# Performance work log

Hardware: AMD Instinct MI355X
Metric: run time of the kernel (lower is better)

## Reference

```python
import jax, jax.numpy as jnp
import numpy as np
from jax import lax

K_NBR = 9  # K nearest neighbors
R = 2      # shuffle_scale


def pixel_unshuffle(x, r):
    B, C, H, W = x.shape
    x = x.reshape(B, C, H // r, r, W // r, r)
    return x.transpose(0, 1, 3, 5, 2, 4).reshape(B, C * r * r, H // r, W // r)


def pixel_shuffle(x, r):
    B, C, H, W = x.shape
    x = x.reshape(B, C // (r * r), r, r, H, W)
    return x.transpose(0, 1, 4, 2, 5, 3).reshape(B, C // (r * r), H * r, W * r)


def conv2d_same(x, w, b):
    y = lax.conv_general_dilated(x, w, (1, 1), 'SAME',
                                 dimension_numbers=('NCHW', 'OIHW', 'NCHW'))
    return y + b[None, :, None, None]


def convnn_branching_layer(x, idx, wa, ba, wb, bb, wp, bp):
    """Conv2d_ConvNN_Random_Branching with shuffle_pattern='BA'."""
    x = pixel_unshuffle(x, R)                      # (B, C*r^2, H/r, W/r)
    B, C, H, W = x.shape
    T = H * W
    # Branch 1: standard 3x3 conv
    y1 = conv2d_same(x, wa, ba)                    # (B, c1, H, W)
    # Branch 2: ConvNN on K nearest of N random samples
    xt = x.reshape(B, C, T)                        # tokens
    samp = xt[:, :, idx]                           # (B, C, N) random samples
    dots = jnp.einsum('bct,bcn->btn', xt, samp)
    xn = jnp.sum(xt * xt, axis=1)[:, :, None]      # (B, T, 1)
    sn = jnp.sum(samp * samp, axis=1)[:, None, :]  # (B, 1, N)
    dist = xn + sn - 2.0 * dots                    # squared euclidean (B, T, N)
    nbr = lax.top_k(-dist, K_NBR)[1]               # (B, T, K) indices into samples
    # gather neighbor features: (B, C, T*K)
    g = jnp.take_along_axis(samp, nbr.reshape(B, 1, T * K_NBR), axis=2)
    g = g.reshape(B, C, T, K_NBR)
    # Conv1d(kernel=K, stride=K) over stacked neighbors
    y2 = jnp.einsum('bctk,ock->bot', g, wb) + bb[None, :, None]
    y2 = y2.reshape(B, wb.shape[0], H, W)          # (B, c2, H, W)
    y = jax.nn.relu(jnp.concatenate([y1, y2], axis=1))
    y = conv2d_same(y, wp, bp)                     # 1x1 -> out*r^2 channels
    return pixel_shuffle(y, R)                     # (B, out, H*r, W*r)


def setup_inputs() -> dict:
    key = jax.random.key(0)
    ks = jax.random.split(key, 24)
    s = 0.02
    B = 256
    inp = {
        'x': jax.random.normal(ks[0], (B, 3, 32, 32), jnp.float32),
        'idx1': jax.random.randint(ks[1], (64,), 0, 256, jnp.int32),
        'idx2': jax.random.randint(ks[2], (64,), 0, 256, jnp.int32),
        # layer 1: Cin = 3*4 = 12, branches 16+16, out 16*4 = 64 pre-shuffle
        'w1a': jax.random.normal(ks[3], (16, 12, 3, 3), jnp.float32) * s,
        'b1a': jnp.zeros((16,), jnp.float32),
        'w1b': jax.random.normal(ks[4], (16, 12, 9), jnp.float32) * s,
        'b1b': jnp.zeros((16,), jnp.float32),
        'w1p': jax.random.normal(ks[5], (64, 32, 1, 1), jnp.float32) * s,
        'b1p': jnp.zeros((64,), jnp.float32),
        # layer 2: Cin = 16*4 = 64, branches 32+32, out 32*4 = 128 pre-shuffle
        'w2a': jax.random.normal(ks[6], (32, 64, 3, 3), jnp.float32) * s,
        'b2a': jnp.zeros((32,), jnp.float32),
        'w2b': jax.random.normal(ks[7], (32, 64, 9), jnp.float32) * s,
        'b2b': jnp.zeros((32,), jnp.float32),
        'w2p': jax.random.normal(ks[8], (128, 64, 1, 1), jnp.float32) * s,
        'b2p': jnp.zeros((128,), jnp.float32),
        # FC head
        'fc1w': jax.random.normal(ks[9], (1024, 32768), jnp.float32) * s,
        'fc1b': jnp.zeros((1024,), jnp.float32),
        'fc2w': jax.random.normal(ks[10], (10, 1024), jnp.float32) * s,
        'fc2b': jnp.zeros((10,), jnp.float32),
    }
    return inp


def reference(x, idx1, idx2, w1a, b1a, w1b, b1b, w1p, b1p,
              w2a, b2a, w2b, b2b, w2p, b2p, fc1w, fc1b, fc2w, fc2b):
    h = convnn_branching_layer(x, idx1, w1a, b1a, w1b, b1b, w1p, b1p)  # (B,16,32,32)
    h = convnn_branching_layer(h, idx2, w2a, b2a, w2b, b2b, w2p, b2p)  # (B,32,32,32)
    h = h.reshape(h.shape[0], -1)                   # (B, 32768)
    h = jax.nn.relu(h @ fc1w.T + fc1b)
    return h @ fc2w.T + fc2b                        # (B, num_classes)
```

## Files before the change

### kernel.cpp

```cpp
#include <hip/hip_runtime.h>
#include <cstdint>
#include <cstddef>


#define DI static __device__ __forceinline__

typedef __attribute__((ext_vector_type(8))) short short8;
typedef __attribute__((ext_vector_type(4))) float f32x4;

DI unsigned short f2bf(float v) {
  unsigned u = __builtin_bit_cast(unsigned, v);
  unsigned r = (u + 0x7FFFu + ((u >> 16) & 1u)) >> 16;
  return (unsigned short)r;
}
DI float bf2f(unsigned short h) {
  unsigned u = ((unsigned)h) << 16;
  return __builtin_bit_cast(float, u);
}

DI float xu1_at(const float* __restrict__ x, int b, int c, int t) {
  int h = t >> 4, w = t & 15;
  return x[(((size_t)b * 3 + (c >> 2)) * 32 + 2 * h + ((c >> 1) & 1)) * 32 + 2 * w + (c & 1)];
}

template <int CIN, bool GATHER, int CCTOT>
__global__ __launch_bounds__(256) void k_conv3x3(
    const float* __restrict__ xsrc, const float* __restrict__ xu,
    const float* __restrict__ w, const float* __restrict__ bias,
    float* __restrict__ ycat)
{
  int b = blockIdx.x;
  int ocb = blockIdx.y * 16;
  __shared__ float xs[CIN * 256];
  int t = threadIdx.x;
  if (GATHER) {
    for (int i = t; i < CIN * 256; i += 256) {
      int c = i >> 8, tt = i & 255;
      xs[i] = xu1_at(xsrc, b, c, tt);
    }
  } else {
    for (int i = t; i < CIN * 256; i += 256) xs[i] = xu[(size_t)b * CIN * 256 + i];
  }
  __syncthreads();
  int h = t >> 4, wc = t & 15;
  float acc[16];
#pragma unroll
  for (int o = 0; o < 16; ++o) acc[o] = bias[ocb + o];
  bool vh0 = h > 0, vh2 = h < 15, vw0 = wc > 0, vw2 = wc < 15;
  bool vm[9] = {vh0 && vw0, vh0, vh0 && vw2, vw0, true, vw2, vh2 && vw0, vh2, vh2 && vw2};
  int tcl[9];
#pragma unroll
  for (int dh = 0; dh < 3; ++dh)
#pragma unroll
    for (int dw = 0; dw < 3; ++dw) {
      int off = (h + dh - 1) * 16 + (wc + dw - 1);
      off = off < 0 ? 0 : (off > 255 ? 255 : off);
      tcl[dh * 3 + dw] = off;
    }
#pragma unroll 2
  for (int ic = 0; ic < CIN; ++ic) {
    float xv[9];
#pragma unroll
    for (int tp = 0; tp < 9; ++tp) {
      float v = xs[ic * 256 + tcl[tp]];
      xv[tp] = vm[tp] ? v : 0.f;
    }
#pragma unroll
    for (int o = 0; o < 16; ++o) {
      const float* wp = w + ((size_t)(ocb + o) * CIN + ic) * 9;
#pragma unroll
      for (int tp = 0; tp < 9; ++tp) acc[o] = fmaf(xv[tp], wp[tp], acc[o]);
    }
  }
#pragma unroll
  for (int o = 0; o < 16; ++o)
    ycat[((size_t)b * CCTOT + ocb + o) * 256 + t] = fmaxf(acc[o], 0.f);
}

__global__ __launch_bounds__(256) void k_prepw(
    const float* __restrict__ w1b, float* __restrict__ wT1,
    const float* __restrict__ w2b, float* __restrict__ wT2)
{
  int t = threadIdx.x;
  for (int i = t; i < 9 * 12 * 16; i += 256) {
    int k = i / (12 * 16), r = i % (12 * 16), c = r >> 4, o = r & 15;
    wT1[i] = w1b[((size_t)o * 12 + c) * 9 + k];
  }
  for (int i = t; i < 9 * 64 * 32; i += 256) {
    int k = i / (64 * 32), r = i % (64 * 32), c = r >> 5, o = r & 31;
    wT2[i] = w2b[((size_t)o * 64 + c) * 9 + k];
  }
}

template <int C, int STR, bool GATHER>
__global__ __launch_bounds__(64) void k_prep(
    const float* __restrict__ xsrc, const float* __restrict__ xu,
    const int* __restrict__ idx,
    float* __restrict__ sampT, float* __restrict__ samp_cn,
    float* __restrict__ snvg)
{
  int b = blockIdx.x, n = threadIdx.x;
  int p = idx[n];
  float s;
  {
#pragma clang fp contract(off)
    s = 0.f;
    for (int c = 0; c < C; ++c) {
      float v = GATHER ? xu1_at(xsrc, b, c, p) : xu[((size_t)b * C + c) * 256 + p];
      sampT[((size_t)b * 64 + n) * STR + c] = v;
      samp_cn[((size_t)b * C + c) * 64 + n] = v;
      s += v * v;
    }
  }
  snvg[(size_t)b * 64 + n] = s;
}

template <int C, int STR, bool GATHER>
__global__ __launch_bounds__(256) void k_nbr(
    const float* __restrict__ xsrc, const float* __restrict__ xu,
    const float* __restrict__ sampT, const float* __restrict__ snvg,
    int* __restrict__ nbr)
{
  int b = blockIdx.x, t = threadIdx.x;
  float xcol[C];
#pragma unroll
  for (int c = 0; c < C; ++c)
    xcol[c] = GATHER ? xu1_at(xsrc, b, c, t) : xu[((size_t)b * C + c) * 256 + t];
  float xn;
  {
#pragma clang fp contract(off)
    xn = 0.f;
#pragma unroll
    for (int c = 0; c < C; ++c) xn += xcol[c] * xcol[c];
  }
  float bd[9];
  int bn[9];
#pragma unroll
  for (int i = 0; i < 9; ++i) { bd[i] = __builtin_inff(); bn[i] = 1 << 30; }

#pragma unroll 1
  for (int n = 0; n < 64; ++n) {
    const float* sp = sampT + ((size_t)b * 64 + n) * STR;
    float snvn = snvg[(size_t)b * 64 + n];
    float d;
    {
#pragma clang fp contract(off)
      float dot = 0.f;
#pragma unroll
      for (int c = 0; c < C; ++c) dot = fmaf(xcol[c], sp[c], dot);
      d = (xn + snvn) - 2.f * dot;
    }
    if (d < bd[8] || (d == bd[8] && n < bn[8])) {
      float dc = d;
      int nc = n;
#pragma unroll
      for (int i = 0; i < 9; ++i) {
        bool sw = (dc < bd[i]) || (dc == bd[i] && nc < bn[i]);
        float ob = bd[i]; int on = bn[i];
        bd[i] = sw ? dc : ob; bn[i] = sw ? nc : on;
        dc = sw ? ob : dc;   nc = sw ? on : nc;
      }
    }
  }
#pragma unroll
  for (int k = 0; k < 9; ++k) nbr[((size_t)b * 9 + k) * 256 + t] = bn[k];
}

template <int C, int OGRP, int OTOT, int CCTOT, int OCBASE>
__global__ __launch_bounds__(256) void k_einsum(
    const float* __restrict__ samp_cn,
    const int* __restrict__ nbr,
    const float* __restrict__ wT,
    const float* __restrict__ bb,
    float* __restrict__ ycat)
{
  int b = blockIdx.x, og = blockIdx.y * OGRP, t = threadIdx.x;
  __shared__ float samps[C * 64];
  for (int i = t; i < C * 64; i += 256)
    samps[i] = samp_cn[(size_t)b * C * 64 + i];
  int bn[9];
#pragma unroll
  for (int k = 0; k < 9; ++k) bn[k] = nbr[((size_t)b * 9 + k) * 256 + t];
  __syncthreads();
  float acc[OGRP];
#pragma unroll
  for (int o = 0; o < OGRP; ++o) acc[o] = bb[og + o];
#pragma unroll 1
  for (int k = 0; k < 9; ++k) {
    int n = bn[k];
    const float* wp = wT + (size_t)k * C * OTOT + og;
#pragma unroll 4
    for (int c = 0; c < C; ++c) {
      float sv = samps[c * 64 + n];
#pragma unroll
      for (int o = 0; o < OGRP; ++o)
        acc[o] = fmaf(sv, wp[c * OTOT + o], acc[o]);
    }
  }
#pragma unroll
  for (int o = 0; o < OGRP; ++o)
    ycat[((size_t)b * CCTOT + OCBASE + og + o) * 256 + t] = fmaxf(acc[o], 0.f);
}

template <int CIN, int OCB, int OCTOT, bool SHUF>
__global__ __launch_bounds__(256) void k_conv1x1(
    const float* __restrict__ yin, const float* __restrict__ w,
    const float* __restrict__ bias, float* __restrict__ out)
{
  int b = blockIdx.x, ocb = blockIdx.y * OCB, t = threadIdx.x;
  __shared__ float ys[CIN * 256];
  for (int i = t; i < CIN * 256; i += 256) ys[i] = yin[(size_t)b * CIN * 256 + i];
  __syncthreads();
  float acc[OCB];
#pragma unroll
  for (int o = 0; o < OCB; ++o) acc[o] = bias[ocb + o];
#pragma unroll 4
  for (int ic = 0; ic < CIN; ++ic) {
    float xv = ys[ic * 256 + t];
#pragma unroll
    for (int o = 0; o < OCB; ++o)
      acc[o] = fmaf(xv, w[(size_t)(ocb + o) * CIN + ic], acc[o]);
  }
  int h = t >> 4, wc = t & 15;
#pragma unroll
  for (int o = 0; o < OCB; ++o) {
    int og = ocb + o;
    if (SHUF) {
      int flat = (og >> 2) * 1024 + (2 * h + ((og >> 1) & 1)) * 32 + (2 * wc + (og & 1));
      out[(size_t)b * 32768 + flat] = acc[o];
    } else {
      out[((size_t)b * OCTOT + og) * 256 + t] = acc[o];
    }
  }
}

__global__ __launch_bounds__(256, 2) void k_fc1(
    const float* __restrict__ A, const float* __restrict__ W,
    float* __restrict__ parts)
{
  constexpr int KTOT = 32768;
  constexpr int LDT = 40;
  __shared__ unsigned short Ah[128 * LDT], Am[128 * LDT], Al[128 * LDT];
  __shared__ unsigned short Wh[128 * LDT], Wm[128 * LDT], Wl[128 * LDT];
  int t = threadIdx.x;
  int nb = blockIdx.x, mb = blockIdx.y, sb = blockIdx.z;
  int m0 = mb * 128, n0 = nb * 128, k0 = sb * 1024;
  int wave = t >> 6, lane = t & 63;
  int q = lane >> 4, m16 = lane & 15;

  f32x4 acc[8][2];
#pragma unroll
  for (int mt = 0; mt < 8; ++mt)
#pragma unroll
    for (int nt = 0; nt < 2; ++nt) acc[mt][nt] = (f32x4){0.f, 0.f, 0.f, 0.f};

  int r8 = t >> 3, c4 = t & 7;

  for (int ks = 0; ks < 1024; ks += 32) {
    int kb = k0 + ks;
    float4 av[4], wv[4];
#pragma unroll
    for (int i = 0; i < 4; ++i) {
      av[i] = *(const float4*)(A + (size_t)(m0 + r8 + 32 * i) * KTOT + kb + c4 * 4);
      wv[i] = *(const float4*)(W + (size_t)(n0 + r8 + 32 * i) * KTOT + kb + c4 * 4);
    }
    __syncthreads();
#pragma unroll
    for (int i = 0; i < 4; ++i) {
      int off = (r8 + 32 * i) * LDT + c4 * 4;
      float vv[4] = {av[i].x, av[i].y, av[i].z, av[i].w};
      ushort4 h4, m4, l4;
      {
        float v = vv[0]; h4.x = f2bf(v); float r1 = v - bf2f(h4.x);
        m4.x = f2bf(r1); l4.x = f2bf(r1 - bf2f(m4.x));
      }
      {
        float v = vv[1]; h4.y = f2bf(v); float r1 = v - bf2f(h4.y);
        m4.y = f2bf(r1); l4.y = f2bf(r1 - bf2f(m4.y));
      }
      {
        float v = vv[2]; h4.z = f2bf(v); float r1 = v - bf2f(h4.z);
        m4.z = f2bf(r1); l4.z = f2bf(r1 - bf2f(m4.z));
      }
      {
        float v = vv[3]; h4.w = f2bf(v); float r1 = v - bf2f(h4.w);
        m4.w = f2bf(r1); l4.w = f2bf(r1 - bf2f(m4.w));
      }
      *(ushort4*)&Ah[off] = h4; *(ushort4*)&Am[off] = m4; *(ushort4*)&Al[off] = l4;
      float uu[4] = {wv[i].x, wv[i].y, wv[i].z, wv[i].w};
      {
        float v = uu[0]; h4.x = f2bf(v); float r1 = v - bf2f(h4.x);
        m4.x = f2bf(r1); l4.x = f2bf(r1 - bf2f(m4.x));
      }
      {
        float v = uu[1]; h4.y = f2bf(v); float r1 = v - bf2f(h4.y);
        m4.y = f2bf(r1); l4.y = f2bf(r1 - bf2f(m4.y));
      }
      {
        float v = uu[2]; h4.z = f2bf(v); float r1 = v - bf2f(h4.z);
        m4.z = f2bf(r1); l4.z = f2bf(r1 - bf2f(m4.z));
      }
      {
        float v = uu[3]; h4.w = f2bf(v); float r1 = v - bf2f(h4.w);
        m4.w = f2bf(r1); l4.w = f2bf(r1 - bf2f(m4.w));
      }
      *(ushort4*)&Wh[off] = h4; *(ushort4*)&Wm[off] = m4; *(ushort4*)&Wl[off] = l4;
    }
    __syncthreads();
    short8 bh[2], bm[2], bl[2];
#pragma unroll
    for (int nt = 0; nt < 2; ++nt) {
      int boff = (wave * 32 + nt * 16 + m16) * LDT + q * 8;
      bh[nt] = *(const short8*)&Wh[boff];
      bm[nt] = *(const short8*)&Wm[boff];
      bl[nt] = *(const short8*)&Wl[boff];
    }
#pragma unroll
    for (int mt = 0; mt < 8; ++mt) {
      int aoff = (mt * 16 + m16) * LDT + q * 8;
      short8 ah = *(const short8*)&Ah[aoff];
      short8 am = *(const short8*)&Am[aoff];
      short8 al = *(const short8*)&Al[aoff];
#pragma unroll
      for (int nt = 0; nt < 2; ++nt) {
        acc[mt][nt] = __builtin_amdgcn_mfma_f32_16x16x32_bf16(al, bh[nt], acc[mt][nt], 0, 0, 0);
        acc[mt][nt] = __builtin_amdgcn_mfma_f32_16x16x32_bf16(am, bm[nt], acc[mt][nt], 0, 0, 0);
        acc[mt][nt] = __builtin_amdgcn_mfma_f32_16x16x32_bf16(ah, bl[nt], acc[mt][nt], 0, 0, 0);
        acc[mt][nt] = __builtin_amdgcn_mfma_f32_16x16x32_bf16(am, bh[nt], acc[mt][nt], 0, 0, 0);
        acc[mt][nt] = __builtin_amdgcn_mfma_f32_16x16x32_bf16(ah, bm[nt], acc[mt][nt], 0, 0, 0);
        acc[mt][nt] = __builtin_amdgcn_mfma_f32_16x16x32_bf16(ah, bh[nt], acc[mt][nt], 0, 0, 0);
      }
    }
  }
  float* P = parts + (size_t)sb * 262144;
#pragma unroll
  for (int mt = 0; mt < 8; ++mt)
#pragma unroll
    for (int nt = 0; nt < 2; ++nt)
#pragma unroll
      for (int r2 = 0; r2 < 4; ++r2) {
        int m = m0 + mt * 16 + q * 4 + r2;
        int n = n0 + wave * 32 + nt * 16 + m16;
        P[(size_t)m * 1024 + n] = acc[mt][nt][r2];
      }
}

__global__ __launch_bounds__(256) void k_fc1_reduce(const float* __restrict__ parts,
                                                    const float* __restrict__ bias,
                                                    float* __restrict__ h1) {
  int i = blockIdx.x * 256 + threadIdx.x;
  float s = 0.f;
#pragma unroll
  for (int sb = 0; sb < 32; ++sb) s += parts[(size_t)sb * 262144 + i];
  h1[i] = fmaxf(s + bias[i & 1023], 0.f);
}

__global__ __launch_bounds__(256) void k_fc2(const float* __restrict__ h1,
                                             const float* __restrict__ w,
                                             const float* __restrict__ bias,
                                             float* __restrict__ out)
{
  int m = blockIdx.x, tid = threadIdx.x;
  __shared__ float hs[1024];
  __shared__ float ps[256];
  for (int i = tid; i < 1024; i += 256) hs[i] = h1[(size_t)m * 1024 + i];
  __syncthreads();
  int n = tid >> 4, sl = tid & 15;
  float p = 0.f;
  if (n < 10) {
    const float* wr = w + (size_t)n * 1024 + sl * 64;
    const float* hr = hs + sl * 64;
#pragma unroll 8
    for (int j = 0; j < 64; ++j) p = fmaf(hr[j], wr[j], p);
  }
  ps[tid] = p;
  __syncthreads();
  if (sl == 0 && n < 10) {
    float s = 0.f;
#pragma unroll
    for (int q = 0; q < 16; ++q) s += ps[n * 16 + q];
    out[(size_t)m * 10 + n] = s + bias[n];
  }
}

extern "C" void kernel_launch(void* const* d_in, const int* in_sizes, int n_in,
                              void* d_out, int out_size, void* d_ws, size_t ws_size,
                              hipStream_t stream) {
  (void)in_sizes; (void)n_in; (void)out_size; (void)ws_size;
  const float* x    = (const float*)d_in[0];
  const int*   idx1 = (const int*)d_in[1];
  const int*   idx2 = (const int*)d_in[2];
  const float* w1a  = (const float*)d_in[3];
  const float* b1a  = (const float*)d_in[4];
  const float* w1b  = (const float*)d_in[5];
  const float* b1b  = (const float*)d_in[6];
  const float* w1p  = (const float*)d_in[7];
  const float* b1p  = (const float*)d_in[8];
  const float* w2a  = (const float*)d_in[9];
  const float* b2a  = (const float*)d_in[10];
  const float* w2b  = (const float*)d_in[11];
  const float* b2b  = (const float*)d_in[12];
  const float* w2p  = (const float*)d_in[13];
  const float* b2p  = (const float*)d_in[14];
  const float* fc1w = (const float*)d_in[15];
  const float* fc1b = (const float*)d_in[16];
  const float* fc2w = (const float*)d_in[17];
  const float* fc2b = (const float*)d_in[18];

  float* ws    = (float*)d_ws;
  float* ycat1 = ws + 0;
  float* xu2   = ws + 2097152;
  float* ycat2 = ws + 6291456;
  float* hshuf = ws + 10485760;
  float* H       = ws + 10485760;
  int*   nbr     = (int*)(H + 0);
  float* sampT1  = H + 589824;
  float* snv1    = H + 851968;
  float* wT1     = H + 868352;
  float* sampT2  = H + 870080;
  float* snv2    = H + 1918656;
  float* wT2     = H + 1935040;
  float* samp_cn1 = H + 1953472;
  float* samp_cn2 = H + 2150080;
  float* parts = ws + 0;
  float* h1    = ws + 8650752;
  float* out   = (float*)d_out;

  k_prepw<<<1, 256, 0, stream>>>(w1b, wT1, w2b, wT2);
  k_conv3x3<12, true, 32><<<dim3(256, 1), 256, 0, stream>>>(x, nullptr, w1a, b1a, ycat1);
  k_prep<12, 16, true><<<256, 64, 0, stream>>>(x, nullptr, idx1, sampT1, samp_cn1, snv1);
  k_nbr<12, 16, true><<<256, 256, 0, stream>>>(x, nullptr, sampT1, snv1, nbr);
  k_einsum<12, 16, 16, 32, 16><<<dim3(256, 1), 256, 0, stream>>>(samp_cn1, nbr, wT1, b1b, ycat1);
  k_conv1x1<32, 64, 64, false><<<dim3(256, 1), 256, 0, stream>>>(ycat1, w1p, b1p, xu2);
  k_conv3x3<64, false, 64><<<dim3(256, 2), 256, 0, stream>>>(nullptr, xu2, w2a, b2a, ycat2);
  k_prep<64, 64, false><<<256, 64, 0, stream>>>(nullptr, xu2, idx2, sampT2, samp_cn2, snv2);
  k_nbr<64, 64, false><<<256, 256, 0, stream>>>(nullptr, xu2, sampT2, snv2, nbr);
  k_einsum<64, 16, 32, 64, 32><<<dim3(256, 2), 256, 0, stream>>>(samp_cn2, nbr, wT2, b2b, ycat2);
  k_conv1x1<64, 64, 128, true><<<dim3(256, 2), 256, 0, stream>>>(ycat2, w2p, b2p, hshuf);
  k_fc1<<<dim3(8, 2, 32), 256, 0, stream>>>(hshuf, fc1w, parts);
  k_fc1_reduce<<<1024, 256, 0, stream>>>(parts, fc1b, h1);
  k_fc2<<<256, 256, 0, stream>>>(h1, fc2w, fc2b, out);
}
```

Baseline: 768.2 us.

## Retile conv, einsum and fc1 kernels with pre-transposed weights and vector loads

Weights for the 3x3, 1x1 and neighbor-einsum stages are pre-transposed so threads can read contiguous float4 weight vectors. Each thread now computes two pixels for a subset of output channels, which doubles weight reuse per load. The sample-gather prep kernel stages samples in shared memory and writes them out with coalesced stores. fc1 shrinks its M tile to 64, drops the W shared-memory staging by splitting W into bf16 pieces directly in registers, and targets three blocks per CU. The risks are extra register pressure and uncoalesced direct W loads in fc1.

After: 692.6 us. 9.8% less time.

```diff
diff --git a/kernel.cpp b/kernel.cpp
--- a/kernel.cpp
+++ b/kernel.cpp
@@ -23,10 +23,47 @@
   return x[(((size_t)b * 3 + (c >> 2)) * 32 + 2 * h + ((c >> 1) & 1)) * 32 + 2 * w + (c & 1)];
 }
 
-template <int CIN, bool GATHER, int CCTOT>
+__global__ __launch_bounds__(256) void k_prepw(
+    const float* __restrict__ w1b, float* __restrict__ wT1,
+    const float* __restrict__ w2b, float* __restrict__ wT2,
+    const float* __restrict__ w1p, float* __restrict__ wp1T,
+    const float* __restrict__ w2p, float* __restrict__ wp2T,
+    const float* __restrict__ w1a, float* __restrict__ wa1T,
+    const float* __restrict__ w2a, float* __restrict__ wa2T)
+{
+  int i = blockIdx.x * 256 + threadIdx.x;
+  if (i < 1728) {
+    int k = i / 192, r = i % 192, c = r >> 4, o = r & 15;
+    wT1[i] = w1b[((size_t)o * 12 + c) * 9 + k];
+    return;
+  }
+  i -= 1728;
+  if (i < 18432) {
+    int k = i / 2048, r = i % 2048, c = r >> 5, o = r & 31;
+    wT2[i] = w2b[((size_t)o * 64 + c) * 9 + k];
+    return;
+  }
+  i -= 18432;
+  if (i < 2048) { int ic = i >> 6, o = i & 63; wp1T[i] = w1p[(size_t)o * 32 + ic]; return; }
+  i -= 2048;
+  if (i < 8192) { int ic = i >> 7, o = i & 127; wp2T[i] = w2p[(size_t)o * 64 + ic]; return; }
+  i -= 8192;
+  if (i < 1728) {
+    int o = i & 15, u = i >> 4, ic = u / 9, tp = u % 9;
+    wa1T[i] = w1a[((size_t)o * 12 + ic) * 9 + tp];
+    return;
+  }
+  i -= 1728;
+  if (i < 18432) {
+    int o = i & 31, u = i >> 5, ic = u / 9, tp = u % 9;
+    wa2T[i] = w2a[((size_t)o * 64 + ic) * 9 + tp];
+  }
+}
+
+template <int CIN, bool GATHER, int CCTOT, int OCT>
 __global__ __launch_bounds__(256) void k_conv3x3(
     const float* __restrict__ xsrc, const float* __restrict__ xu,
-    const float* __restrict__ w, const float* __restrict__ bias,
+    const float* __restrict__ waT, const float* __restrict__ bias,
     float* __restrict__ ycat)
 {
   int b = blockIdx.x;
@@ -42,77 +79,87 @@
     for (int i = t; i < CIN * 256; i += 256) xs[i] = xu[(size_t)b * CIN * 256 + i];
   }
   __syncthreads();
-  int h = t >> 4, wc = t & 15;
-  float acc[16];
-#pragma unroll
-  for (int o = 0; o < 16; ++o) acc[o] = bias[ocb + o];
-  bool vh0 = h > 0, vh2 = h < 15, vw0 = wc > 0, vw2 = wc < 15;
-  bool vm[9] = {vh0 && vw0, vh0, vh0 && vw2, vw0, true, vw2, vh2 && vw0, vh2, vh2 && vw2};
-  int tcl[9];
+  int tt = t & 127, og = t >> 7;
+  int oc0 = ocb + og * 8;
+  int h0 = tt >> 4, wc = tt & 15;
+  float acc0[8], acc1[8];
+#pragma unroll
+  for (int o = 0; o < 8; ++o) { acc0[o] = bias[oc0 + o]; acc1[o] = acc0[o]; }
+  bool vw0 = wc > 0, vw2 = wc < 15, vh0 = h0 > 0, vh7 = h0 < 7;
+  bool m0v[9] = {vh0 && vw0, vh0, vh0 && vw2, vw0, true, vw2, vw0, true, vw2};
+  bool m1v[9] = {vw0, true, vw2, vw0, true, vw2, vh7 && vw0, vh7, vh7 && vw2};
+  int tc0[9], tc1[9];
 #pragma unroll
   for (int dh = 0; dh < 3; ++dh)
 #pragma unroll
     for (int dw = 0; dw < 3; ++dw) {
-      int off = (h + dh - 1) * 16 + (wc + dw - 1);
-      off = off < 0 ? 0 : (off > 255 ? 255 : off);
-      tcl[dh * 3 + dw] = off;
+      int o0 = (h0 + dh - 1) * 16 + (wc + dw - 1);
+      int o1 = (h0 + 8 + dh - 1) * 16 + (wc + dw - 1);
+      tc0[dh * 3 + dw] = o0 < 0 ? 0 : (o0 > 255 ? 255 : o0);
+      tc1[dh * 3 + dw] = o1 < 0 ? 0 : (o1 > 255 ? 255 : o1);
     }
 #pragma unroll 2
   for (int ic = 0; ic < CIN; ++ic) {
-    float xv[9];
+    float xv0[9], xv1[9];
 #pragma unroll
     for (int tp = 0; tp < 9; ++tp) {
-      float v = xs[ic * 256 + tcl[tp]];
-      xv[tp] = vm[tp] ? v : 0.f;
-    }
-#pragma unroll
-    for (int o = 0; o < 16; ++o) {
-      const float* wp = w + ((size_t)(ocb + o) * CIN + ic) * 9;
-#pragma unroll
-      for (int tp = 0; tp < 9; ++tp) acc[o] = fmaf(xv[tp], wp[tp], acc[o]);
-    }
-  }
-#pragma unroll
-  for (int o = 0; o < 16; ++o)
-    ycat[((size_t)b * CCTOT + ocb + o) * 256 + t] = fmaxf(acc[o], 0.f);
-}
-
-__global__ __launch_bounds__(256) void k_prepw(
-    const float* __restrict__ w1b, float* __restrict__ wT1,
-    const float* __restrict__ w2b, float* __restrict__ wT2)
-{
-  int t = threadIdx.x;
-  for (int i = t; i < 9 * 12 * 16; i += 256) {
-    int k = i / (12 * 16), r = i % (12 * 16), c = r >> 4, o = r & 15;
-    wT1[i] = w1b[((size_t)o * 12 + c) * 9 + k];
-  }
-  for (int i = t; i < 9 * 64 * 32; i += 256) {
-    int k = i / (64 * 32), r = i % (64 * 32), c = r >> 5, o = r & 31;
-    wT2[i] = w2b[((size_t)o * 64 + c) * 9 + k];
+      float v0 = xs[ic * 256 + tc0[tp]];
+      float v1 = xs[ic * 256 + tc1[tp]];
+      xv0[tp] = m0v[tp] ? v0 : 0.f;
+      xv1[tp] = m1v[tp] ? v1 : 0.f;
+    }
+#pragma unroll
+    for (int tp = 0; tp < 9; ++tp) {
+      const float* wp = waT + ((size_t)ic * 9 + tp) * OCT + oc0;
+      float4 wA = *(const float4*)wp;
+      float4 wB = *(const float4*)(wp + 4);
+      float wv[8] = {wA.x, wA.y, wA.z, wA.w, wB.x, wB.y, wB.z, wB.w};
+#pragma unroll
+      for (int o = 0; o < 8; ++o) {
+        acc0[o] = fmaf(xv0[tp], wv[o], acc0[o]);
+        acc1[o] = fmaf(xv1[tp], wv[o], acc1[o]);
+      }
+    }
+  }
+#pragma unroll
+  for (int o = 0; o < 8; ++o) {
+    ycat[((size_t)b * CCTOT + oc0 + o) * 256 + tt] = fmaxf(acc0[o], 0.f);
+    ycat[((size_t)b * CCTOT + oc0 + o) * 256 + tt + 128] = fmaxf(acc1[o], 0.f);
   }
 }
 
 template <int C, int STR, bool GATHER>
-__global__ __launch_bounds__(64) void k_prep(
+__global__ __launch_bounds__(256) void k_prep(
     const float* __restrict__ xsrc, const float* __restrict__ xu,
     const int* __restrict__ idx,
     float* __restrict__ sampT, float* __restrict__ samp_cn,
     float* __restrict__ snvg)
 {
-  int b = blockIdx.x, n = threadIdx.x;
-  int p = idx[n];
-  float s;
-  {
+  int b = blockIdx.x, t = threadIdx.x;
+  __shared__ float sph[C * 64];
+  __shared__ int idxs[64];
+  if (t < 64) idxs[t] = idx[t];
+  __syncthreads();
+  for (int i = t; i < C * 64; i += 256) {
+    int c = i >> 6, n = i & 63;
+    int p = idxs[n];
+    sph[i] = GATHER ? xu1_at(xsrc, b, c, p) : xu[((size_t)b * C + c) * 256 + p];
+  }
+  __syncthreads();
+  for (int i = t; i < C * 64; i += 256) samp_cn[(size_t)b * C * 64 + i] = sph[i];
+  for (int i = t; i < 64 * STR; i += 256) {
+    int n = i / STR, c = i % STR;
+    if (c < C) sampT[(size_t)b * 64 * STR + i] = sph[c * 64 + n];
+  }
+  if (t < 64) {
+    float s;
+    {
 #pragma clang fp contract(off)
-    s = 0.f;
-    for (int c = 0; c < C; ++c) {
-      float v = GATHER ? xu1_at(xsrc, b, c, p) : xu[((size_t)b * C + c) * 256 + p];
-      sampT[((size_t)b * 64 + n) * STR + c] = v;
-      samp_cn[((size_t)b * C + c) * 64 + n] = v;
-      s += v * v;
-    }
-  }
-  snvg[(size_t)b * 64 + n] = s;
+      s = 0.f;
+      for (int c = 0; c < C; ++c) { float v = sph[c * 64 + t]; s += v * v; }
+    }
+    snvg[(size_t)b * 64 + t] = s;
+  }
 }
 
 template <int C, int STR, bool GATHER>
@@ -166,7 +213,7 @@
   for (int k = 0; k < 9; ++k) nbr[((size_t)b * 9 + k) * 256 + t] = bn[k];
 }
 
-template <int C, int OGRP, int OTOT, int CCTOT, int OCBASE>
+template <int C, int OPT, int OTOT, int CCTOT, int OCBASE>
 __global__ __launch_bounds__(256) void k_einsum(
     const float* __restrict__ samp_cn,
     const int* __restrict__ nbr,
@@ -174,149 +221,169 @@
     const float* __restrict__ bb,
     float* __restrict__ ycat)
 {
-  int b = blockIdx.x, og = blockIdx.y * OGRP, t = threadIdx.x;
+  int b = blockIdx.x, t = threadIdx.x;
+  int tt = t & 127, og = t >> 7;
+  int o0 = og * OPT;
   __shared__ float samps[C * 64];
   for (int i = t; i < C * 64; i += 256)
     samps[i] = samp_cn[(size_t)b * C * 64 + i];
-  int bn[9];
-#pragma unroll
-  for (int k = 0; k < 9; ++k) bn[k] = nbr[((size_t)b * 9 + k) * 256 + t];
-  __syncthreads();
-  float acc[OGRP];
-#pragma unroll
-  for (int o = 0; o < OGRP; ++o) acc[o] = bb[og + o];
+  int bnA[9], bnB[9];
+#pragma unroll
+  for (int k = 0; k < 9; ++k) {
+    bnA[k] = nbr[((size_t)b * 9 + k) * 256 + tt];
+    bnB[k] = nbr[((size_t)b * 9 + k) * 256 + tt + 128];
+  }
+  __syncthreads();
+  float acc0[OPT], acc1[OPT];
+#pragma unroll
+  for (int o = 0; o < OPT; ++o) { acc0[o] = bb[o0 + o]; acc1[o] = acc0[o]; }
 #pragma unroll 1
   for (int k = 0; k < 9; ++k) {
-    int n = bn[k];
-    const float* wp = wT + (size_t)k * C * OTOT + og;
-#pragma unroll 4
+    int n0 = bnA[k], n1 = bnB[k];
+#pragma unroll 2
     for (int c = 0; c < C; ++c) {
-      float sv = samps[c * 64 + n];
-#pragma unroll
-      for (int o = 0; o < OGRP; ++o)
-        acc[o] = fmaf(sv, wp[c * OTOT + o], acc[o]);
-    }
-  }
-#pragma unroll
-  for (int o = 0; o < OGRP; ++o)
-    ycat[((size_t)b * CCTOT + OCBASE + og + o) * 256 + t] = fmaxf(acc[o], 0.f);
-}
-
-template <int CIN, int OCB, int OCTOT, bool SHUF>
+      float sv0 = samps[c * 64 + n0];
+      float sv1 = samps[c * 64 + n1];
+      const float* wp = wT + ((size_t)k * C + c) * OTOT + o0;
+#pragma unroll
+      for (int oq = 0; oq < OPT / 4; ++oq) {
+        float4 wv = ((const float4*)wp)[oq];
+        float w4[4] = {wv.x, wv.y, wv.z, wv.w};
+#pragma unroll
+        for (int j = 0; j < 4; ++j) {
+          acc0[oq * 4 + j] = fmaf(sv0, w4[j], acc0[oq * 4 + j]);
+          acc1[oq * 4 + j] = fmaf(sv1, w4[j], acc1[oq * 4 + j]);
+        }
+      }
+    }
+  }
+#pragma unroll
+  for (int o = 0; o < OPT; ++o) {
+    ycat[((size_t)b * CCTOT + OCBASE + o0 + o) * 256 + tt] = fmaxf(acc0[o], 0.f);
+    ycat[((size_t)b * CCTOT + OCBASE + o0 + o) * 256 + tt + 128] = fmaxf(acc1[o], 0.f);
+  }
+}
+
+template <int CIN, int OPT, int OCTOT, bool SHUF>
 __global__ __launch_bounds__(256) void k_conv1x1(
-    const float* __restrict__ yin, const float* __restrict__ w,
+    const float* __restrict__ yin, const float* __restrict__ wpT,
     const float* __restrict__ bias, float* __restrict__ out)
 {
-  int b = blockIdx.x, ocb = blockIdx.y * OCB, t = threadIdx.x;
+  int b = blockIdx.x, ocb = blockIdx.y * 2 * OPT, t = threadIdx.x;
+  int tt = t & 127, og = t >> 7;
+  int o0 = ocb + og * OPT;
   __shared__ float ys[CIN * 256];
   for (int i = t; i < CIN * 256; i += 256) ys[i] = yin[(size_t)b * CIN * 256 + i];
   __syncthreads();
-  float acc[OCB];
-#pragma unroll
-  for (int o = 0; o < OCB; ++o) acc[o] = bias[ocb + o];
-#pragma unroll 4
+  float acc0[OPT], acc1[OPT];
+#pragma unroll
+  for (int o = 0; o < OPT; ++o) { acc0[o] = bias[o0 + o]; acc1[o] = acc0[o]; }
+#pragma unroll 2
   for (int ic = 0; ic < CIN; ++ic) {
-    float xv = ys[ic * 256 + t];
-#pragma unroll
-    for (int o = 0; o < OCB; ++o)
-      acc[o] = fmaf(xv, w[(size_t)(ocb + o) * CIN + ic], acc[o]);
-  }
-  int h = t >> 4, wc = t & 15;
-#pragma unroll
-  for (int o = 0; o < OCB; ++o) {
-    int og = ocb + o;
+    float sv0 = ys[ic * 256 + tt];
+    float sv1 = ys[ic * 256 + tt + 128];
+    const float* wp = wpT + (size_t)ic * OCTOT + o0;
+#pragma unroll
+    for (int oq = 0; oq < OPT / 4; ++oq) {
+      float4 wv = ((const float4*)wp)[oq];
+      float w4[4] = {wv.x, wv.y, wv.z, wv.w};
+#pragma unroll
+      for (int j = 0; j < 4; ++j) {
+        acc0[oq * 4 + j] = fmaf(sv0, w4[j], acc0[oq * 4 + j]);
+        acc1[oq * 4 + j] = fmaf(sv1, w4[j], acc1[oq * 4 + j]);
+      }
+    }
+  }
+  int h0 = tt >> 4, wc = tt & 15;
+#pragma unroll
+  for (int o = 0; o < OPT; ++o) {
+    int ogl = o0 + o;
     if (SHUF) {
-      int flat = (og >> 2) * 1024 + (2 * h + ((og >> 1) & 1)) * 32 + (2 * wc + (og & 1));
-      out[(size_t)b * 32768 + flat] = acc[o];
+      int f0 = (ogl >> 2) * 1024 + (2 * h0 + ((ogl >> 1) & 1)) * 32 + (2 * wc + (ogl & 1));
+      int f1 = (ogl >> 2) * 1024 + (2 * (h0 + 8) + ((ogl >> 1) & 1)) * 32 + (2 * wc + (ogl & 1));
+      out[(size_t)b * 32768 + f0] = acc0[o];
+      out[(size_t)b * 32768 + f1] = acc1[o];
     } else {
-      out[((size_t)b * OCTOT + og) * 256 + t] = acc[o];
-    }
-  }
-}
-
-__global__ __launch_bounds__(256, 2) void k_fc1(
+      out[((size_t)b * OCTOT + ogl) * 256 + tt] = acc0[o];
+      out[((size_t)b * OCTOT + ogl) * 256 + tt + 128] = acc1[o];
+    }
+  }
+}
+
+__global__ __launch_bounds__(256, 3) void k_fc1(
     const float* __restrict__ A, const float* __restrict__ W,
     float* __restrict__ parts)
 {
   constexpr int KTOT = 32768;
   constexpr int LDT = 40;
-  __shared__ unsigned short Ah[128 * LDT], Am[128 * LDT], Al[128 * LDT];
-  __shared__ unsigned short Wh[128 * LDT], Wm[128 * LDT], Wl[128 * LDT];
+  __shared__ unsigned short Ah[64 * LDT], Am[64 * LDT], Al[64 * LDT];
   int t = threadIdx.x;
   int nb = blockIdx.x, mb = blockIdx.y, sb = blockIdx.z;
-  int m0 = mb * 128, n0 = nb * 128, k0 = sb * 1024;
+  int m0 = mb * 64, n0 = nb * 128, k0 = sb * 1024;
   int wave = t >> 6, lane = t & 63;
   int q = lane >> 4, m16 = lane & 15;
 
-  f32x4 acc[8][2];
-#pragma unroll
-  for (int mt = 0; mt < 8; ++mt)
+  f32x4 acc[4][2];
+#pragma unroll
+  for (int mt = 0; mt < 4; ++mt)
 #pragma unroll
     for (int nt = 0; nt < 2; ++nt) acc[mt][nt] = (f32x4){0.f, 0.f, 0.f, 0.f};
 
   int r8 = t >> 3, c4 = t & 7;
+  const float* A0 = A + (size_t)(m0 + r8) * KTOT + k0 + c4 * 4;
+  const float* A1 = A + (size_t)(m0 + r8 + 32) * KTOT + k0 + c4 * 4;
+  const float* W0 = W + (size_t)(n0 + wave * 32 + m16) * KTOT + k0 + q * 8;
+  const float* W1 = W + (size_t)(n0 + wave * 32 + 16 + m16) * KTOT + k0 + q * 8;
 
   for (int ks = 0; ks < 1024; ks += 32) {
-    int kb = k0 + ks;
-    float4 av[4], wv[4];
-#pragma unroll
-    for (int i = 0; i < 4; ++i) {
-      av[i] = *(const float4*)(A + (size_t)(m0 + r8 + 32 * i) * KTOT + kb + c4 * 4);
-      wv[i] = *(const float4*)(W + (size_t)(n0 + r8 + 32 * i) * KTOT + kb + c4 * 4);
-    }
+    float4 a0 = *(const float4*)(A0 + ks);
+    float4 a1 = *(const float4*)(A1 + ks);
+    float4 w0a = *(const float4*)(W0 + ks), w0b = *(const float4*)(W0 + ks + 4);
+    float4 w1a = *(const float4*)(W1 + ks), w1b = *(const float4*)(W1 + ks + 4);
     __syncthreads();
-#pragma unroll
-    for (int i = 0; i < 4; ++i) {
-      int off = (r8 + 32 * i) * LDT + c4 * 4;
-      float vv[4] = {av[i].x, av[i].y, av[i].z, av[i].w};
+    {
+      float vv[8] = {a0.x, a0.y, a0.z, a0.w, a1.x, a1.y, a1.z, a1.w};
+      int off0 = r8 * LDT + c4 * 4, off1 = (r8 + 32) * LDT + c4 * 4;
       ushort4 h4, m4, l4;
-      {
-        float v = vv[0]; h4.x = f2bf(v); float r1 = v - bf2f(h4.x);
-        m4.x = f2bf(r1); l4.x = f2bf(r1 - bf2f(m4.x));
-      }
-      {
-        float v = vv[1]; h4.y = f2bf(v); float r1 = v - bf2f(h4.y);
-        m4.y = f2bf(r1); l4.y = f2bf(r1 - bf2f(m4.y));
-      }
-      {
-        float v = vv[2]; h4.z = f2bf(v); float r1 = v - bf2f(h4.z);
-        m4.z = f2bf(r1); l4.z = f2bf(r1 - bf2f(m4.z));
-      }
-      {
-        float v = vv[3]; h4.w = f2bf(v); float r1 = v - bf2f(h4.w);
-        m4.w = f2bf(r1); l4.w = f2bf(r1 - bf2f(m4.w));
-      }
-      *(ushort4*)&Ah[off] = h4; *(ushort4*)&Am[off] = m4; *(ushort4*)&Al[off] = l4;
-      float uu[4] = {wv[i].x, wv[i].y, wv[i].z, wv[i].w};
-      {
-        float v = uu[0]; h4.x = f2bf(v); float r1 = v - bf2f(h4.x);
-        m4.x = f2bf(r1); l4.x = f2bf(r1 - bf2f(m4.x));
-      }
-      {
-        float v = uu[1]; h4.y = f2bf(v); float r1 = v - bf2f(h4.y);
-        m4.y = f2bf(r1); l4.y = f2bf(r1 - bf2f(m4.y));
-      }
-      {
-        float v = uu[2]; h4.z = f2bf(v); float r1 = v - bf2f(h4.z);
-        m4.z = f2bf(r1); l4.z = f2bf(r1 - bf2f(m4.z));
-      }
-      {
-        float v = uu[3]; h4.w = f2bf(v); float r1 = v - bf2f(h4.w);
-        m4.w = f2bf(r1); l4.w = f2bf(r1 - bf2f(m4.w));
-      }
-      *(ushort4*)&Wh[off] = h4; *(ushort4*)&Wm[off] = m4; *(ushort4*)&Wl[off] = l4;
+#pragma unroll
+      for (int g = 0; g < 2; ++g) {
+        {
+          float v = vv[g * 4 + 0]; h4.x = f2bf(v); float r1 = v - bf2f(h4.x);
+          m4.x = f2bf(r1); l4.x = f2bf(r1 - bf2f(m4.x));
+        }
+        {
+          float v = vv[g * 4 + 1]; h4.y = f2bf(v); float r1 = v - bf2f(h4.y);
+          m4.y = f2bf(r1); l4.y = f2bf(r1 - bf2f(m4.y));
+        }
+        {
+          float v = vv[g * 4 + 2]; h4.z = f2bf(v); float r1 = v - bf2f(h4.z);
+          m4.z = f2bf(r1); l4.z = f2bf(r1 - bf2f(m4.z));
+        }
+        {
+          float v = vv[g * 4 + 3]; h4.w = f2bf(v); float r1 = v - bf2f(h4.w);
+          m4.w = f2bf(r1); l4.w = f2bf(r1 - bf2f(m4.w));
+        }
+        int off = g == 0 ? off0 : off1;
+        *(ushort4*)&Ah[off] = h4; *(ushort4*)&Am[off] = m4; *(ushort4*)&Al[off] = l4;
+      }
     }
     __syncthreads();
     short8 bh[2], bm[2], bl[2];
-#pragma unroll
-    for (int nt = 0; nt < 2; ++nt) {
-      int boff = (wave * 32 + nt * 16 + m16) * LDT + q * 8;
-      bh[nt] = *(const short8*)&Wh[boff];
-      bm[nt] = *(const short8*)&Wm[boff];
-      bl[nt] = *(const short8*)&Wl[boff];
-    }
-#pragma unroll
-    for (int mt = 0; mt < 8; ++mt) {
+    {
+      float wf0[8] = {w0a.x, w0a.y, w0a.z, w0a.w, w0b.x, w0b.y, w0b.z, w0b.w};
+      float wf1[8] = {w1a.x, w1a.y, w1a.z, w1a.w, w1b.x, w1b.y, w1b.z, w1b.w};
+#pragma unroll
+      for (int j = 0; j < 8; ++j) {
+        unsigned short h = f2bf(wf0[j]); float r1 = wf0[j] - bf2f(h);
+        unsigned short m = f2bf(r1);
+        bh[0][j] = (short)h; bm[0][j] = (short)m; bl[0][j] = (short)f2bf(r1 - bf2f(m));
+        h = f2bf(wf1[j]); r1 = wf1[j] - bf2f(h);
+        m = f2bf(r1);
+        bh[1][j] = (short)h; bm[1][j] = (short)m; bl[1][j] = (short)f2bf(r1 - bf2f(m));
+      }
+    }
+#pragma unroll
+    for (int mt = 0; mt < 4; ++mt) {
       int aoff = (mt * 16 + m16) * LDT + q * 8;
       short8 ah = *(const short8*)&Ah[aoff];
       short8 am = *(const short8*)&Am[aoff];
@@ -334,7 +401,7 @@
   }
   float* P = parts + (size_t)sb * 262144;
 #pragma unroll
-  for (int mt = 0; mt < 8; ++mt)
+  for (int mt = 0; mt < 4; ++mt)
 #pragma unroll
     for (int nt = 0; nt < 2; ++nt)
 #pragma unroll
@@ -408,36 +475,41 @@
   const float* fc2b = (const float*)d_in[18];
 
   float* ws    = (float*)d_ws;
-  float* ycat1 = ws + 0;
-  float* xu2   = ws + 2097152;
-  float* ycat2 = ws + 6291456;
+  float* xu2   = ws + 0;
+  float* ycat1 = ws + 4194304;
+  float* ycat2 = ws + 4194304;
+  float* WGT   = ws + 8388608;
+  float* wT1   = WGT + 0;
+  float* wT2   = WGT + 1728;
+  float* wp1T  = WGT + 20160;
+  float* wp2T  = WGT + 22208;
+  float* wa1T  = WGT + 30400;
+  float* wa2T  = WGT + 32128;
+  float* h1    = ws + 8650752;
   float* hshuf = ws + 10485760;
-  float* H       = ws + 10485760;
-  int*   nbr     = (int*)(H + 0);
-  float* sampT1  = H + 589824;
-  float* snv1    = H + 851968;
-  float* wT1     = H + 868352;
-  float* sampT2  = H + 870080;
-  float* snv2    = H + 1918656;
-  float* wT2     = H + 1935040;
-  float* samp_cn1 = H + 1953472;
-  float* samp_cn2 = H + 2150080;
+  float* H        = ws + 10485760;
+  int*   nbr      = (int*)(H + 0);
+  float* sampT1   = H + 589824;
+  float* snv1     = H + 851968;
+  float* sampT2   = H + 868352;
+  float* snv2     = H + 1916928;
+  float* samp_cn1 = H + 1933312;
+  float* samp_cn2 = H + 2129920;
   float* parts = ws + 0;
-  float* h1    = ws + 8650752;
   float* out   = (float*)d_out;
 
-  k_prepw<<<1, 256, 0, stream>>>(w1b, wT1, w2b, wT2);
-  k_conv3x3<12, true, 32><<<dim3(256, 1), 256, 0, stream>>>(x, nullptr, w1a, b1a, ycat1);
-  k_prep<12, 16, true><<<256, 64, 0, stream>>>(x, nullptr, idx1, sampT1, samp_cn1, snv1);
+  k_prepw<<<198, 256, 0, stream>>>(w1b, wT1, w2b, wT2, w1p, wp1T, w2p, wp2T, w1a, wa1T, w2a, wa2T);
+  k_conv3x3<12, true, 32, 16><<<dim3(256, 1), 256, 0, stream>>>(x, nullptr, wa1T, b1a, ycat1);
+  k_prep<12, 16, true><<<256, 256, 0, stream>>>(x, nullptr, idx1, sampT1, samp_cn1, snv1);
   k_nbr<12, 16, true><<<256, 256, 0, stream>>>(x, nullptr, sampT1, snv1, nbr);
-  k_einsum<12, 16, 16, 32, 16><<<dim3(256, 1), 256, 0, stream>>>(samp_cn1, nbr, wT1, b1b, ycat1);
-  k_conv1x1<32, 64, 64, false><<<dim3(256, 1), 256, 0, stream>>>(ycat1, w1p, b1p, xu2);
-  k_conv3x3<64, false, 64><<<dim3(256, 2), 256, 0, stream>>>(nullptr, xu2, w2a, b2a, ycat2);
-  k_prep<64, 64, false><<<256, 64, 0, stream>>>(nullptr, xu2, idx2, sampT2, samp_cn2, snv2);
+  k_einsum<12, 8, 16, 32, 16><<<256, 256, 0, stream>>>(samp_cn1, nbr, wT1, b1b, ycat1);
+  k_conv1x1<32, 32, 64, false><<<dim3(256, 1), 256, 0, stream>>>(ycat1, wp1T, b1p, xu2);
+  k_conv3x3<64, false, 64, 32><<<dim3(256, 2), 256, 0, stream>>>(nullptr, xu2, wa2T, b2a, ycat2);
+  k_prep<64, 64, false><<<256, 256, 0, stream>>>(nullptr, xu2, idx2, sampT2, samp_cn2, snv2);
   k_nbr<64, 64, false><<<256, 256, 0, stream>>>(nullptr, xu2, sampT2, snv2, nbr);
-  k_einsum<64, 16, 32, 64, 32><<<dim3(256, 2), 256, 0, stream>>>(samp_cn2, nbr, wT2, b2b, ycat2);
-  k_conv1x1<64, 64, 128, true><<<dim3(256, 2), 256, 0, stream>>>(ycat2, w2p, b2p, hshuf);
-  k_fc1<<<dim3(8, 2, 32), 256, 0, stream>>>(hshuf, fc1w, parts);
+  k_einsum<64, 16, 32, 64, 32><<<256, 256, 0, stream>>>(samp_cn2, nbr, wT2, b2b, ycat2);
+  k_conv1x1<64, 32, 128, true><<<dim3(256, 2), 256, 0, stream>>>(ycat2, wp2T, b2p, hshuf);
+  k_fc1<<<dim3(8, 4, 32), 256, 0, stream>>>(hshuf, fc1w, parts);
   k_fc1_reduce<<<1024, 256, 0, stream>>>(parts, fc1b, h1);
   k_fc2<<<256, 256, 0, stream>>>(h1, fc2w, fc2b, out);
 }
```
